# Performance work log

Hardware: AMD Instinct MI355X
Metric: run time of the kernel (lower is better)

The kernel has to match this reference:

```python
import jax, jax.numpy as jnp
import numpy as np

_N = 2048          # matrix_size (A_sparse.shape[0] in the original)
_NNZ = 32768       # number of factor / pred entries
_LOGCOND_EPS = 1e-12


def setup_inputs() -> dict:
    key = jax.random.key(0)
    k1, k2, k3, k4, k5 = jax.random.split(key, 5)
    pred_values = jax.random.normal(k1, (_NNZ,), dtype=jnp.float32)
    active_scales = jax.random.uniform(k2, (_NNZ,), dtype=jnp.float32) * 0.05
    A_factor = jax.random.normal(k3, (_N, _N), dtype=jnp.float32)
    factor_rows = jax.random.randint(k4, (_NNZ,), 0, _N, dtype=jnp.int32)
    factor_cols = jax.random.randint(k5, (_NNZ,), 0, _N, dtype=jnp.int32)
    return {
        "pred_values": pred_values,
        "active_scales": active_scales,
        "A_factor": A_factor,
        "factor_rows": factor_rows,
        "factor_cols": factor_cols,
    }


def reference(pred_values, active_scales, A_factor, factor_rows, factor_cols):
    n = A_factor.shape[0]
    dt = pred_values.dtype
    # SPD system matrix A (stands in for the original fixed A_sparse)
    A = A_factor @ A_factor.T / jnp.asarray(n, dt) + jnp.eye(n, dtype=dt)
    # Sparse factor L assembled from predicted values (scatter-add, dup-safe),
    # unit diagonal keeps L A L^T well conditioned / SPD.
    L = jnp.eye(n, dtype=dt).at[factor_rows, factor_cols].add(pred_values * active_scales)
    # Preconditioned matrix M = L A L^T (symmetric PSD)
    M = L @ A @ L.T
    M = 0.5 * (M + M.T)
    evals = jnp.linalg.eigvalsh(M)  # ascending
    lam_min = jnp.maximum(evals[0], _LOGCOND_EPS)
    lam_max = jnp.maximum(evals[-1], _LOGCOND_EPS)
    # loss = log(lambda_max) - log(lambda_min) = log condition number
    return jnp.log(lam_max) - jnp.log(lam_min)
```

## Files before the change

### kernel.cpp

```cpp
#include <hip/hip_runtime.h>

#define N2 2048
#define NNZ 32768
#define LK 22
#define NBL 128
#define BINCAP 64

typedef __attribute__((ext_vector_type(8))) _Float16 half8;
typedef __attribute__((ext_vector_type(4))) float f32x4;

#define AGENT __HIP_MEMORY_SCOPE_AGENT
#define AS1C(p) ((const __attribute__((address_space(1))) unsigned int*)(p))
#define AS3(p)  ((__attribute__((address_space(3))) unsigned int*)(p))

__device__ __forceinline__ unsigned short f2h(float f) {
  _Float16 h = (_Float16)f;
  return *(unsigned short*)&h;
}


__global__ __launch_bounds__(256) void convert_kernel(const float* __restrict__ W,
                                                      unsigned short* __restrict__ Hf,
                                                      unsigned* __restrict__ cntR,
                                                      unsigned* __restrict__ cntC) {
  if (blockIdx.x < 8)       cntR[blockIdx.x * 256 + threadIdx.x] = 0;
  else if (blockIdx.x < 16) cntC[(blockIdx.x - 8) * 256 + threadIdx.x] = 0;
  int i4 = blockIdx.x * 256 + threadIdx.x;
  float4 w = ((const float4*)W)[i4];
  ushort4 h;
  h.x = f2h(w.x); h.y = f2h(w.y); h.z = f2h(w.z); h.w = f2h(w.w);
  ((ushort4*)Hf)[i4] = h;
}

__global__ __launch_bounds__(256) void fill_kernel(const float* __restrict__ pred,
                                                   const float* __restrict__ scal,
                                                   const int* __restrict__ rows,
                                                   const int* __restrict__ cols,
                                                   unsigned* __restrict__ cntR,
                                                   int* __restrict__ binRc,
                                                   float* __restrict__ binRv,
                                                   unsigned* __restrict__ cntC,
                                                   int* __restrict__ binCr,
                                                   float* __restrict__ binCv) {
  int k = blockIdx.x * 256 + threadIdx.x;
  int r = rows[k], c = cols[k];
  float v = pred[k] * scal[k];
  unsigned pR = atomicAdd(&cntR[r], 1u);
  if (pR < BINCAP) { binRc[r * BINCAP + pR] = c; binRv[r * BINCAP + pR] = v; }
  unsigned pC = atomicAdd(&cntC[c], 1u);
  if (pC < BINCAP) { binCr[c * BINCAP + pC] = r; binCv[c * BINCAP + pC] = v; }
}

__global__ __launch_bounds__(256) void gatherG_kernel(const unsigned* __restrict__ cntR,
                                                      const int* __restrict__ binRc,
                                                      const float* __restrict__ binRv,
                                                      const unsigned short* __restrict__ Hf,
                                                      unsigned short* __restrict__ Gh) {
  const int r = blockIdx.x, tid = threadIdx.x;
  __shared__ int scol_[BINCAP];
  __shared__ float sval_[BINCAP];
  const unsigned ne = min(cntR[r], (unsigned)BINCAP);
  if (tid < ne) {
    scol_[tid] = binRc[r * BINCAP + tid];
    sval_[tid] = binRv[r * BINCAP + tid];
  }
  __syncthreads();
  uint4 own = *(const uint4*)(Hf + (size_t)r * 2048 + tid * 8);
  half8 ho = *(half8*)&own;
  float acc[8];
#pragma unroll
  for (int k = 0; k < 8; ++k) acc[k] = (float)ho[k];
  unsigned e = 0;
  for (; e + 8 <= ne; e += 8) {
    uint4 q[8];
#pragma unroll
    for (int u = 0; u < 8; ++u)
      q[u] = *(const uint4*)(Hf + (size_t)scol_[e + u] * 2048 + tid * 8);
#pragma unroll
    for (int u = 0; u < 8; ++u) {
      half8 hv = *(half8*)&q[u];
      const float v = sval_[e + u];
#pragma unroll
      for (int k = 0; k < 8; ++k) acc[k] += v * (float)hv[k];
    }
  }
  for (; e + 4 <= ne; e += 4) {
    uint4 q[4];
#pragma unroll
    for (int u = 0; u < 4; ++u)
      q[u] = *(const uint4*)(Hf + (size_t)scol_[e + u] * 2048 + tid * 8);
#pragma unroll
    for (int u = 0; u < 4; ++u) {
      half8 hv = *(half8*)&q[u];
      const float v = sval_[e + u];
#pragma unroll
      for (int k = 0; k < 8; ++k) acc[k] += v * (float)hv[k];
    }
  }
  for (; e < ne; ++e) {
    uint4 qq = *(const uint4*)(Hf + (size_t)scol_[e] * 2048 + tid * 8);
    half8 hv = *(half8*)&qq;
    const float v = sval_[e];
#pragma unroll
    for (int k = 0; k < 8; ++k) acc[k] += v * (float)hv[k];
  }
  unsigned short o[8];
#pragma unroll
  for (int k = 0; k < 8; ++k) o[k] = f2h(acc[k]);
  *(uint4*)(Gh + (size_t)r * 2048 + tid * 8) = *(uint4*)o;
}

__device__ __forceinline__ void stageXY(const unsigned short* __restrict__ Gh,
                                        char* Xb, char* Yb,
                                        int row0, int col0, int k0,
                                        int w, int lane) {
  const int srcc = ((lane & 7) * 16) ^ ((lane >> 3) << 4);
#pragma unroll
  for (int q = 0; q < 2; ++q) {
    const int rl = w * 16 + q * 8 + (lane >> 3);
    __builtin_amdgcn_global_load_lds(
        AS1C((const char*)(Gh + (size_t)(row0 + rl) * 2048 + k0) + srcc),
        AS3(Xb + (w * 16 + q * 8) * 128), 16, 0, 0);
    __builtin_amdgcn_global_load_lds(
        AS1C((const char*)(Gh + (size_t)(col0 + rl) * 2048 + k0) + srcc),
        AS3(Yb + (w * 16 + q * 8) * 128), 16, 0, 0);
  }
}

__global__ __launch_bounds__(512) void gemmM_kernel(const unsigned short* __restrict__ Gh,
                                                    float* __restrict__ M) {
  const int tid = threadIdx.x;
  int bi, bj;
  bool diag;
  if (blockIdx.x < 16) {
    bi = bj = blockIdx.x; diag = true;
  } else {
    int idx = blockIdx.x - 16;
    int j = 0;
    while (j < 15) {
      int offn = 15 * (j + 1) - (j + 1) * j / 2;
      if (idx < offn) break;
      ++j;
    }
    bj = j;
    int off = 15 * j - j * (j - 1) / 2;
    bi = j + 1 + (idx - off);
    diag = false;
  }

  __shared__ __align__(16) char smem[65536];
  float* LDSf = (float*)smem;

  const int w = tid >> 6, lane = tid & 63;
  const int row0 = bi * 128, col0 = bj * 128;
  const int mrow = lane & 15;
  const int crow = (lane >> 4) * 4, ccol = lane & 15;
  f32x4 acc[8];
#pragma unroll
  for (int n = 0; n < 8; ++n) acc[n] = (f32x4){0.f, 0.f, 0.f, 0.f};

  stageXY(Gh, smem, smem + 32768, row0, col0, 0, w, lane);

  const int arow = w * 16 + mrow;
  const int xswA = (mrow & 7) << 4;
  for (int t = 0; t < 32; ++t) {
    __syncthreads();
    if (t < 31)
      stageXY(Gh, smem + ((t + 1) & 1) * 16384, smem + 32768 + ((t + 1) & 1) * 16384,
              row0, col0, (t + 1) * 64, w, lane);
    const char* Xb = smem + (t & 1) * 16384;
    const char* Yb = smem + 32768 + (t & 1) * 16384;
#pragma unroll
    for (int kk = 0; kk < 2; ++kk) {
      const int cb = kk * 64 + (lane >> 4) * 16;
      half8 af = *(const half8*)(Xb + arow * 128 + (cb ^ xswA));
#pragma unroll
      for (int nt = 0; nt < 8; ++nt) {
        const int nrow = nt * 16 + mrow;
        half8 bf = *(const half8*)(Yb + nrow * 128 + (cb ^ ((nrow & 7) << 4)));
        acc[nt] = __builtin_amdgcn_mfma_f32_16x16x32_f16(af, bf, acc[nt], 0, 0, 0);
      }
    }
  }
  const float invn = 1.0f / 2048.0f;
  float vals[8][4];
#pragma unroll
  for (int nt = 0; nt < 8; ++nt) {
    const int gj = col0 + nt * 16 + ccol;
#pragma unroll
    for (int r = 0; r < 4; ++r) {
      const int gi = row0 + w * 16 + crow + r;
      float v = acc[nt][r] * invn + ((gi == gj) ? 1.0f : 0.0f);
      vals[nt][r] = v;
      M[(size_t)gi * 2048 + gj] = v;
    }
  }
  if (!diag) {
    __syncthreads();
    for (int round = 0; round < 2; ++round) {
      if ((w >> 2) == round) {
        float* myc = LDSf + (w & 3) * (16 * 132);
#pragma unroll
        for (int nt = 0; nt < 8; ++nt)
#pragma unroll
          for (int r = 0; r < 4; ++r)
            myc[(crow + r) * 132 + nt * 16 + ccol] = vals[nt][r];
        for (int u = 0; u < 32; ++u) {
          const int jj = u * 4 + (lane >> 4);
          const int ii = lane & 15;
          M[(size_t)(col0 + jj) * 2048 + row0 + w * 16 + ii] = myc[ii * 132 + jj];
        }
      }
      __syncthreads();
    }
  }
}

__device__ __forceinline__ float block_sum8(float v, float* red) {
#pragma unroll
  for (int off = 32; off; off >>= 1) v += __shfl_down(v, off);
  if ((threadIdx.x & 63) == 0) red[threadIdx.x >> 6] = v;
  __syncthreads();
  float r = ((red[0] + red[1]) + (red[2] + red[3])) +
            ((red[4] + red[5]) + (red[6] + red[7]));
  __syncthreads();
  return r;
}

__global__ __launch_bounds__(512) void lanczos_kernel(const float* __restrict__ M,
                                                      const unsigned* __restrict__ cntR,
                                                      const int* __restrict__ binRc,
                                                      const float* __restrict__ binRv,
                                                      const unsigned* __restrict__ cntC,
                                                      const int* __restrict__ binCr,
                                                      const float* __restrict__ binCv,
                                                      unsigned long long* __restrict__ Z0,
                                                      unsigned long long* __restrict__ Z1,
                                                      float* __restrict__ out) {
  const int tid = threadIdx.x, b = blockIdx.x;
  const int wave = tid >> 6, lane = tid & 63;
  __shared__ __align__(16) float Mlds[16 * 2048];
  __shared__ __align__(16) float VA[2048];
  __shared__ __align__(16) float VB[2048];
  __shared__ float red[8];
  __shared__ float al[LK + 2], b2[LK + 2];
  __shared__ float bnds[2], res[2];

  const float* Mblk = M + (size_t)b * 16 * 2048;
#pragma unroll
  for (int q = 0; q < 16; ++q)
    __builtin_amdgcn_global_load_lds(AS1C(Mblk + wave * 4096 + q * 256 + lane * 4),
                                     AS3(Mlds + wave * 4096 + q * 256), 16, 0, 0);

  float pv[4];
  float part = 0.f;
#pragma unroll
  for (int t = 0; t < 4; ++t) {
    int i = t * 512 + tid;
    unsigned u = (unsigned)i * 2654435761u;
    u ^= u >> 16; u *= 2246822519u; u ^= u >> 13;
    float rv = (float)(u >> 8) * (2.f / 16777216.f) - 1.f;
    pv[t] = rv;
    part += rv * rv;
  }
  float nrm = block_sum8(part, red);
  float innm = rsqrtf(nrm);
#pragma unroll
  for (int t = 0; t < 4; ++t) {
    int i = t * 512 + tid;
    VA[i] = pv[t] * innm;
    VB[i] = 0.f;
  }
  __syncthreads();

  for (int rr = 0; rr < 2; ++rr) {
    const int r = b * 16 + wave * 2 + rr;
    float* Mrow = Mlds + (wave * 2 + rr) * 2048;
    const unsigned nR = min(cntR[r], (unsigned)BINCAP);
    const unsigned nC = min(cntC[r], (unsigned)BINCAP);
    int c_ = 0; float v_ = 0.f; unsigned n_ = 0;
    if (lane < nR) {
      c_ = binRc[r * BINCAP + lane];
      v_ = binRv[r * BINCAP + lane];
      n_ = min(cntC[c_], (unsigned)BINCAP);
    }
    if (lane < nR) atomicAdd(&Mrow[c_], v_);
    if (lane < nC)
      atomicAdd(&Mrow[binCr[r * BINCAP + lane]], binCv[r * BINCAP + lane]);
    const unsigned g = lane >> 4, p0 = lane & 15;
    for (unsigned e = g; e < nR; e += 4) {
      const int c = __shfl(c_, (int)e);
      const float v = __shfl(v_, (int)e);
      const unsigned n2 = __shfl(n_, (int)e);
      for (unsigned p = p0; p < n2; p += 16)
        atomicAdd(&Mrow[binCr[c * BINCAP + p]], v * binCv[c * BINCAP + p]);
    }
  }
  __syncthreads();

  float* Vcur = VA;
  float* Vprev = VB;
  float beta_prev = 0.f;

  for (int j = 1; j <= LK; ++j) {
    unsigned long long* Z = (j & 1) ? Z0 : Z1;
#pragma unroll
    for (int rr = 0; rr < 2; ++rr) {
      const int r = b * 16 + wave * 2 + rr;
      const float4* Mr = (const float4*)(Mlds + (wave * 2 + rr) * 2048);
      float s = 0.f;
#pragma unroll
      for (int t = 0; t < 8; ++t) {
        int idx = t * 64 + lane;
        float4 m4 = Mr[idx];
        float4 v4 = ((const float4*)Vcur)[idx];
        s += m4.x * v4.x + m4.y * v4.y + m4.z * v4.z + m4.w * v4.w;
      }
#pragma unroll
      for (int off = 32; off; off >>= 1) s += __shfl_down(s, off);
      if (lane == 0) {
        float zv = s - beta_prev * Vprev[r];
        unsigned long long pk = ((unsigned long long)(unsigned)j << 32) |
                                (unsigned long long)(unsigned)__float_as_uint(zv);
        __hip_atomic_store(&Z[r], pk, __ATOMIC_RELAXED, AGENT);
      }
    }

    float va[4];
#pragma unroll
    for (int t = 0; t < 4; ++t) va[t] = Vcur[t * 512 + tid];

    unsigned long long w4[4];
    int rounds = 0;
    for (;;) {
      bool ok = true;
#pragma unroll
      for (int t = 0; t < 4; ++t) {
        w4[t] = __hip_atomic_load(&Z[t * 512 + tid], __ATOMIC_RELAXED, AGENT);
        ok &= ((unsigned)(w4[t] >> 32) == (unsigned)j);
      }
      if (ok) break;
      if (rounds == 1)      __builtin_amdgcn_s_sleep(1);
      else if (rounds == 2) __builtin_amdgcn_s_sleep(2);
      else if (rounds >= 3) __builtin_amdgcn_s_sleep(8);
      ++rounds;
    }
    float za[4];
    float pa = 0.f;
#pragma unroll
    for (int t = 0; t < 4; ++t) {
      za[t] = __uint_as_float((unsigned)w4[t]);
      pa += za[t] * va[t];
    }
    float alpha = block_sum8(pa, red);
    float pb = 0.f;
#pragma unroll
    for (int t = 0; t < 4; ++t) {
      float rsd = za[t] - alpha * va[t];
      pb += rsd * rsd;
    }
    float beta2 = block_sum8(pb, red);
    float beta = sqrtf(fmaxf(beta2, 1e-30f));
    float invb = 1.f / beta;
    if (tid == 0) { al[j] = alpha; b2[j] = beta2; }
#pragma unroll
    for (int t = 0; t < 4; ++t) {
      int i = t * 512 + tid;
      Vprev[i] = (za[t] - alpha * va[t]) * invb;
    }
    float* tmp = Vprev; Vprev = Vcur; Vcur = tmp;
    beta_prev = beta;
    __syncthreads();
  }

  if (b == 0) {
    if (tid == 0) {
      float lo = 1e30f, hi = -1e30f;
      for (int i = 1; i <= LK; ++i) {
        float bl = (i > 1) ? sqrtf(b2[i - 1]) : 0.f;
        float br = (i < LK) ? sqrtf(b2[i]) : 0.f;
        lo = fminf(lo, al[i] - bl - br);
        hi = fmaxf(hi, al[i] + bl + br);
      }
      bnds[0] = lo; bnds[1] = hi;
    }
    __syncthreads();
    if (wave < 2) {
      const int tcount = (wave == 0) ? 1 : LK;
      float lo = bnds[0], hi = bnds[1];
      for (int round = 0; round < 4; ++round) {
        float x = lo + (hi - lo) * (float)(lane + 1) * (1.f / 65.f);
        int cnt = 0;
        float d = al[1] - x;
        if (fabsf(d) < 1e-25f) d = -1e-25f;
        if (d < 0.f) cnt++;
        for (int i = 2; i <= LK; ++i) {
          d = (al[i] - x) - b2[i - 1] / d;
          if (fabsf(d) < 1e-25f) d = -1e-25f;
          if (d < 0.f) cnt++;
        }
        bool ab = (cnt >= tcount);
        float cand_hi = ab ? x : hi;
        float cand_lo = ab ? lo : x;
#pragma unroll
        for (int off = 32; off; off >>= 1) {
          cand_hi = fminf(cand_hi, __shfl_down(cand_hi, off));
          cand_lo = fmaxf(cand_lo, __shfl_down(cand_lo, off));
        }
        cand_hi = __shfl(cand_hi, 0);
        cand_lo = __shfl(cand_lo, 0);
        hi = cand_hi;
        lo = fminf(cand_lo, hi);
      }
      if (lane == 0) res[wave] = 0.5f * (lo + hi);
    }
    __syncthreads();
    if (tid == 0) {
      float lmin = fmaxf(res[0], 1e-12f);
      float lmax = fmaxf(res[1], 1e-12f);
      out[0] = logf(lmax) - logf(lmin);
    }
  }
}

extern "C" void kernel_launch(void* const* d_in, const int* in_sizes, int n_in,
                              void* d_out, int out_size, void* d_ws, size_t ws_size,
                              hipStream_t stream) {
  const float* pred = (const float*)d_in[0];
  const float* scal = (const float*)d_in[1];
  const float* W    = (const float*)d_in[2];
  const int*   rows = (const int*)d_in[3];
  const int*   cols = (const int*)d_in[4];
  float* out = (float*)d_out;

  char* ws = (char*)d_ws;
  const size_t MB = 1024 * 1024;
  unsigned short* Hf = (unsigned short*)(ws);
  unsigned short* Gh = (unsigned short*)(ws + 8 * MB);
  float* M = (float*)(ws + 16 * MB);
  char* ctrl = ws + 32 * MB;
  unsigned* cntR = (unsigned*)(ctrl);
  unsigned* cntC = (unsigned*)(ctrl + 8192);
  int*      binRc = (int*)(ctrl + 16384);
  float*    binRv = (float*)(ctrl + 16384 + 524288);
  int*      binCr = (int*)(ctrl + 16384 + 2 * 524288);
  float*    binCv = (float*)(ctrl + 16384 + 3 * 524288);
  unsigned long long* Z0 = (unsigned long long*)(ctrl + 16384 + 4 * 524288);
  unsigned long long* Z1 = (unsigned long long*)(ctrl + 16384 + 4 * 524288 + 16384);

  convert_kernel<<<4096, 256, 0, stream>>>(W, Hf, cntR, cntC);
  fill_kernel<<<NNZ / 256, 256, 0, stream>>>(pred, scal, rows, cols,
                                             cntR, binRc, binRv, cntC, binCr, binCv);
  gatherG_kernel<<<2048, 256, 0, stream>>>(cntR, binRc, binRv, Hf, Gh);
  gemmM_kernel<<<136, 512, 0, stream>>>(Gh, M);
  lanczos_kernel<<<NBL, 512, 0, stream>>>(M, cntR, binRc, binRv,
                                          cntC, binCr, binCv, Z0, Z1, out);
}
```

Before: 245.4 us.

## Fuse all five stages into one cooperative persistent kernel with grid syncs

Replaces the five separate launches (convert, bin fill, sparse gather, MFMA GEMM, Lanczos) with a single cooperative kernel of 256 blocks that runs each stage in turn, separated by grid.sync(). The intent is to remove per-launch overhead and inter-kernel gaps. In exchange, the convert and gather stages run at lower parallelism (8 rows per block instead of one block per row), and every block carries the large Lanczos LDS allocation, which limits occupancy for the early stages. Cooperative launch also requires that all 256 blocks be resident at once.

```diff
diff --git a/kernel.cpp b/kernel.cpp
--- a/kernel.cpp
+++ b/kernel.cpp
@@ -1,9 +1,11 @@
 #include <hip/hip_runtime.h>
+#include <hip/hip_cooperative_groups.h>
+
+namespace cg = cooperative_groups;
 
 #define N2 2048
 #define NNZ 32768
 #define LK 22
-#define NBL 128
 #define BINCAP 64
 
 typedef __attribute__((ext_vector_type(8))) _Float16 half8;
@@ -18,97 +20,6 @@
   return *(unsigned short*)&h;
 }
 
-
-__global__ __launch_bounds__(256) void convert_kernel(const float* __restrict__ W,
-                                                      unsigned short* __restrict__ Hf,
-                                                      unsigned* __restrict__ cntR,
-                                                      unsigned* __restrict__ cntC) {
-  if (blockIdx.x < 8)       cntR[blockIdx.x * 256 + threadIdx.x] = 0;
-  else if (blockIdx.x < 16) cntC[(blockIdx.x - 8) * 256 + threadIdx.x] = 0;
-  int i4 = blockIdx.x * 256 + threadIdx.x;
-  float4 w = ((const float4*)W)[i4];
-  ushort4 h;
-  h.x = f2h(w.x); h.y = f2h(w.y); h.z = f2h(w.z); h.w = f2h(w.w);
-  ((ushort4*)Hf)[i4] = h;
-}
-
-__global__ __launch_bounds__(256) void fill_kernel(const float* __restrict__ pred,
-                                                   const float* __restrict__ scal,
-                                                   const int* __restrict__ rows,
-                                                   const int* __restrict__ cols,
-                                                   unsigned* __restrict__ cntR,
-                                                   int* __restrict__ binRc,
-                                                   float* __restrict__ binRv,
-                                                   unsigned* __restrict__ cntC,
-                                                   int* __restrict__ binCr,
-                                                   float* __restrict__ binCv) {
-  int k = blockIdx.x * 256 + threadIdx.x;
-  int r = rows[k], c = cols[k];
-  float v = pred[k] * scal[k];
-  unsigned pR = atomicAdd(&cntR[r], 1u);
-  if (pR < BINCAP) { binRc[r * BINCAP + pR] = c; binRv[r * BINCAP + pR] = v; }
-  unsigned pC = atomicAdd(&cntC[c], 1u);
-  if (pC < BINCAP) { binCr[c * BINCAP + pC] = r; binCv[c * BINCAP + pC] = v; }
-}
-
-__global__ __launch_bounds__(256) void gatherG_kernel(const unsigned* __restrict__ cntR,
-                                                      const int* __restrict__ binRc,
-                                                      const float* __restrict__ binRv,
-                                                      const unsigned short* __restrict__ Hf,
-                                                      unsigned short* __restrict__ Gh) {
-  const int r = blockIdx.x, tid = threadIdx.x;
-  __shared__ int scol_[BINCAP];
-  __shared__ float sval_[BINCAP];
-  const unsigned ne = min(cntR[r], (unsigned)BINCAP);
-  if (tid < ne) {
-    scol_[tid] = binRc[r * BINCAP + tid];
-    sval_[tid] = binRv[r * BINCAP + tid];
-  }
-  __syncthreads();
-  uint4 own = *(const uint4*)(Hf + (size_t)r * 2048 + tid * 8);
-  half8 ho = *(half8*)&own;
-  float acc[8];
-#pragma unroll
-  for (int k = 0; k < 8; ++k) acc[k] = (float)ho[k];
-  unsigned e = 0;
-  for (; e + 8 <= ne; e += 8) {
-    uint4 q[8];
-#pragma unroll
-    for (int u = 0; u < 8; ++u)
-      q[u] = *(const uint4*)(Hf + (size_t)scol_[e + u] * 2048 + tid * 8);
-#pragma unroll
-    for (int u = 0; u < 8; ++u) {
-      half8 hv = *(half8*)&q[u];
-      const float v = sval_[e + u];
-#pragma unroll
-      for (int k = 0; k < 8; ++k) acc[k] += v * (float)hv[k];
-    }
-  }
-  for (; e + 4 <= ne; e += 4) {
-    uint4 q[4];
-#pragma unroll
-    for (int u = 0; u < 4; ++u)
-      q[u] = *(const uint4*)(Hf + (size_t)scol_[e + u] * 2048 + tid * 8);
-#pragma unroll
-    for (int u = 0; u < 4; ++u) {
-      half8 hv = *(half8*)&q[u];
-      const float v = sval_[e + u];
-#pragma unroll
-      for (int k = 0; k < 8; ++k) acc[k] += v * (float)hv[k];
-    }
-  }
-  for (; e < ne; ++e) {
-    uint4 qq = *(const uint4*)(Hf + (size_t)scol_[e] * 2048 + tid * 8);
-    half8 hv = *(half8*)&qq;
-    const float v = sval_[e];
-#pragma unroll
-    for (int k = 0; k < 8; ++k) acc[k] += v * (float)hv[k];
-  }
-  unsigned short o[8];
-#pragma unroll
-  for (int k = 0; k < 8; ++k) o[k] = f2h(acc[k]);
-  *(uint4*)(Gh + (size_t)r * 2048 + tid * 8) = *(uint4*)o;
-}
 
 __device__ __forceinline__ void stageXY(const unsigned short* __restrict__ Gh,
                                         char* Xb, char* Yb,
@@ -127,95 +38,6 @@
   }
 }
 
-__global__ __launch_bounds__(512) void gemmM_kernel(const unsigned short* __restrict__ Gh,
-                                                    float* __restrict__ M) {
-  const int tid = threadIdx.x;
-  int bi, bj;
-  bool diag;
-  if (blockIdx.x < 16) {
-    bi = bj = blockIdx.x; diag = true;
-  } else {
-    int idx = blockIdx.x - 16;
-    int j = 0;
-    while (j < 15) {
-      int offn = 15 * (j + 1) - (j + 1) * j / 2;
-      if (idx < offn) break;
-      ++j;
-    }
-    bj = j;
-    int off = 15 * j - j * (j - 1) / 2;
-    bi = j + 1 + (idx - off);
-    diag = false;
-  }
-
-  __shared__ __align__(16) char smem[65536];
-  float* LDSf = (float*)smem;
-
-  const int w = tid >> 6, lane = tid & 63;
-  const int row0 = bi * 128, col0 = bj * 128;
-  const int mrow = lane & 15;
-  const int crow = (lane >> 4) * 4, ccol = lane & 15;
-  f32x4 acc[8];
-#pragma unroll
-  for (int n = 0; n < 8; ++n) acc[n] = (f32x4){0.f, 0.f, 0.f, 0.f};
-
-  stageXY(Gh, smem, smem + 32768, row0, col0, 0, w, lane);
-
-  const int arow = w * 16 + mrow;
-  const int xswA = (mrow & 7) << 4;
-  for (int t = 0; t < 32; ++t) {
-    __syncthreads();
-    if (t < 31)
-      stageXY(Gh, smem + ((t + 1) & 1) * 16384, smem + 32768 + ((t + 1) & 1) * 16384,
-              row0, col0, (t + 1) * 64, w, lane);
-    const char* Xb = smem + (t & 1) * 16384;
-    const char* Yb = smem + 32768 + (t & 1) * 16384;
-#pragma unroll
-    for (int kk = 0; kk < 2; ++kk) {
-      const int cb = kk * 64 + (lane >> 4) * 16;
-      half8 af = *(const half8*)(Xb + arow * 128 + (cb ^ xswA));
-#pragma unroll
-      for (int nt = 0; nt < 8; ++nt) {
-        const int nrow = nt * 16 + mrow;
-        half8 bf = *(const half8*)(Yb + nrow * 128 + (cb ^ ((nrow & 7) << 4)));
-        acc[nt] = __builtin_amdgcn_mfma_f32_16x16x32_f16(af, bf, acc[nt], 0, 0, 0);
-      }
-    }
-  }
-  const float invn = 1.0f / 2048.0f;
-  float vals[8][4];
-#pragma unroll
-  for (int nt = 0; nt < 8; ++nt) {
-    const int gj = col0 + nt * 16 + ccol;
-#pragma unroll
-    for (int r = 0; r < 4; ++r) {
-      const int gi = row0 + w * 16 + crow + r;
-      float v = acc[nt][r] * invn + ((gi == gj) ? 1.0f : 0.0f);
-      vals[nt][r] = v;
-      M[(size_t)gi * 2048 + gj] = v;
-    }
-  }
-  if (!diag) {
-    __syncthreads();
-    for (int round = 0; round < 2; ++round) {
-      if ((w >> 2) == round) {
-        float* myc = LDSf + (w & 3) * (16 * 132);
-#pragma unroll
-        for (int nt = 0; nt < 8; ++nt)
-#pragma unroll
-          for (int r = 0; r < 4; ++r)
-            myc[(crow + r) * 132 + nt * 16 + ccol] = vals[nt][r];
-        for (int u = 0; u < 32; ++u) {
-          const int jj = u * 4 + (lane >> 4);
-          const int ii = lane & 15;
-          M[(size_t)(col0 + jj) * 2048 + row0 + w * 16 + ii] = myc[ii * 132 + jj];
-        }
-      }
-      __syncthreads();
-    }
-  }
-}
-
 __device__ __forceinline__ float block_sum8(float v, float* red) {
 #pragma unroll
   for (int off = 32; off; off >>= 1) v += __shfl_down(v, off);
@@ -227,24 +49,198 @@
   return r;
 }
 
-__global__ __launch_bounds__(512) void lanczos_kernel(const float* __restrict__ M,
-                                                      const unsigned* __restrict__ cntR,
-                                                      const int* __restrict__ binRc,
-                                                      const float* __restrict__ binRv,
-                                                      const unsigned* __restrict__ cntC,
-                                                      const int* __restrict__ binCr,
-                                                      const float* __restrict__ binCv,
-                                                      unsigned long long* __restrict__ Z0,
-                                                      unsigned long long* __restrict__ Z1,
-                                                      float* __restrict__ out) {
+__global__ __launch_bounds__(512) void mega_kernel(
+    const float* __restrict__ W, const float* __restrict__ pred,
+    const float* __restrict__ scal, const int* __restrict__ rows,
+    const int* __restrict__ cols,
+    unsigned short* __restrict__ Hf, unsigned short* __restrict__ Gh,
+    float* __restrict__ M,
+    unsigned* __restrict__ cntR, int* __restrict__ binRc, float* __restrict__ binRv,
+    unsigned* __restrict__ cntC, int* __restrict__ binCr, float* __restrict__ binCv,
+    unsigned long long* __restrict__ Z0, unsigned long long* __restrict__ Z1,
+    float* __restrict__ out) {
+  cg::grid_group grid = cg::this_grid();
   const int tid = threadIdx.x, b = blockIdx.x;
+  const int gid = b * 512 + tid;
   const int wave = tid >> 6, lane = tid & 63;
+
   __shared__ __align__(16) float Mlds[16 * 2048];
   __shared__ __align__(16) float VA[2048];
   __shared__ __align__(16) float VB[2048];
   __shared__ float red[8];
-  __shared__ float al[LK + 2], b2[LK + 2];
+  __shared__ float al[LK + 2], b2v[LK + 2];
   __shared__ float bnds[2], res[2];
+
+  if (gid < 2048)            cntR[gid] = 0;
+  else if (gid < 4096)       cntC[gid - 2048] = 0;
+  for (int i4 = gid; i4 < 1048576; i4 += 131072) {
+    float4 w4 = ((const float4*)W)[i4];
+    ushort4 h;
+    h.x = f2h(w4.x); h.y = f2h(w4.y); h.z = f2h(w4.z); h.w = f2h(w4.w);
+    ((ushort4*)Hf)[i4] = h;
+  }
+  grid.sync();
+
+  if (gid < NNZ) {
+    int r = rows[gid], c = cols[gid];
+    float v = pred[gid] * scal[gid];
+    unsigned pR = atomicAdd(&cntR[r], 1u);
+    if (pR < BINCAP) { binRc[r * BINCAP + pR] = c; binRv[r * BINCAP + pR] = v; }
+    unsigned pC = atomicAdd(&cntC[c], 1u);
+    if (pC < BINCAP) { binCr[c * BINCAP + pC] = r; binCv[c * BINCAP + pC] = v; }
+  }
+  grid.sync();
+
+  {
+    int* sc_ = (int*)VA;
+    float* sv_ = (float*)VB;
+    for (int it = 0; it < 4; ++it) {
+      const int sub = tid >> 8;
+      const int t2 = tid & 255;
+      const int r = b * 8 + it * 2 + sub;
+      int* sc = sc_ + sub * BINCAP;
+      float* sv = sv_ + sub * BINCAP;
+      const unsigned ne = min(cntR[r], (unsigned)BINCAP);
+      if (t2 < (int)ne) {
+        sc[t2] = binRc[r * BINCAP + t2];
+        sv[t2] = binRv[r * BINCAP + t2];
+      }
+      __syncthreads();
+      uint4 own = *(const uint4*)(Hf + (size_t)r * 2048 + t2 * 8);
+      half8 ho = *(half8*)&own;
+      float acc[8];
+#pragma unroll
+      for (int k = 0; k < 8; ++k) acc[k] = (float)ho[k];
+      unsigned e = 0;
+      for (; e + 8 <= ne; e += 8) {
+        uint4 q[8];
+#pragma unroll
+        for (int u = 0; u < 8; ++u)
+          q[u] = *(const uint4*)(Hf + (size_t)sc[e + u] * 2048 + t2 * 8);
+#pragma unroll
+        for (int u = 0; u < 8; ++u) {
+          half8 hv = *(half8*)&q[u];
+          const float v = sv[e + u];
+#pragma unroll
+          for (int k = 0; k < 8; ++k) acc[k] += v * (float)hv[k];
+        }
+      }
+      for (; e + 4 <= ne; e += 4) {
+        uint4 q[4];
+#pragma unroll
+        for (int u = 0; u < 4; ++u)
+          q[u] = *(const uint4*)(Hf + (size_t)sc[e + u] * 2048 + t2 * 8);
+#pragma unroll
+        for (int u = 0; u < 4; ++u) {
+          half8 hv = *(half8*)&q[u];
+          const float v = sv[e + u];
+#pragma unroll
+          for (int k = 0; k < 8; ++k) acc[k] += v * (float)hv[k];
+        }
+      }
+      for (; e < ne; ++e) {
+        uint4 qq = *(const uint4*)(Hf + (size_t)sc[e] * 2048 + t2 * 8);
+        half8 hv = *(half8*)&qq;
+        const float v = sv[e];
+#pragma unroll
+        for (int k = 0; k < 8; ++k) acc[k] += v * (float)hv[k];
+      }
+      unsigned short o[8];
+#pragma unroll
+      for (int k = 0; k < 8; ++k) o[k] = f2h(acc[k]);
+      *(uint4*)(Gh + (size_t)r * 2048 + t2 * 8) = *(uint4*)o;
+      __syncthreads();
+    }
+  }
+  grid.sync();
+
+  if (b < 136) {
+    char* smem = (char*)Mlds;
+    float* LDSf = (float*)smem;
+    int bi, bj;
+    bool diag;
+    if (b < 16) {
+      bi = bj = b; diag = true;
+    } else {
+      int idx = b - 16;
+      int j = 0;
+      while (j < 15) {
+        int offn = 15 * (j + 1) - (j + 1) * j / 2;
+        if (idx < offn) break;
+        ++j;
+      }
+      bj = j;
+      int off = 15 * j - j * (j - 1) / 2;
+      bi = j + 1 + (idx - off);
+      diag = false;
+    }
+    const int w = wave;
+    const int row0 = bi * 128, col0 = bj * 128;
+    const int mrow = lane & 15;
+    const int crow = (lane >> 4) * 4, ccol = lane & 15;
+    const int arow = w * 16 + mrow;
+    const int xswA = (mrow & 7) << 4;
+    f32x4 acc[8];
+#pragma unroll
+    for (int n = 0; n < 8; ++n) acc[n] = (f32x4){0.f, 0.f, 0.f, 0.f};
+
+    stageXY(Gh, smem, smem + 32768, row0, col0, 0, w, lane);
+    for (int t = 0; t < 32; ++t) {
+      __syncthreads();
+      if (t < 31)
+        stageXY(Gh, smem + ((t + 1) & 1) * 16384,
+                smem + 32768 + ((t + 1) & 1) * 16384,
+                row0, col0, (t + 1) * 64, w, lane);
+      const char* Xb = smem + (t & 1) * 16384;
+      const char* Yb = smem + 32768 + (t & 1) * 16384;
+#pragma unroll
+      for (int kk = 0; kk < 2; ++kk) {
+        const int cb = kk * 64 + (lane >> 4) * 16;
+        half8 af = *(const half8*)(Xb + arow * 128 + (cb ^ xswA));
+#pragma unroll
+        for (int nt = 0; nt < 8; ++nt) {
+          const int nrow = nt * 16 + mrow;
+          half8 bf = *(const half8*)(Yb + nrow * 128 + (cb ^ ((nrow & 7) << 4)));
+          acc[nt] = __builtin_amdgcn_mfma_f32_16x16x32_f16(af, bf, acc[nt], 0, 0, 0);
+        }
+      }
+    }
+    const float invn = 1.0f / 2048.0f;
+    float vals[8][4];
+#pragma unroll
+    for (int nt = 0; nt < 8; ++nt) {
+      const int gj = col0 + nt * 16 + ccol;
+#pragma unroll
+      for (int r = 0; r < 4; ++r) {
+        const int gi = row0 + w * 16 + crow + r;
+        float v = acc[nt][r] * invn + ((gi == gj) ? 1.0f : 0.0f);
+        vals[nt][r] = v;
+        M[(size_t)gi * 2048 + gj] = v;
+      }
+    }
+    if (!diag) {
+      __syncthreads();
+      for (int round = 0; round < 2; ++round) {
+        if ((w >> 2) == round) {
+          float* myc = LDSf + (w & 3) * (16 * 132);
+#pragma unroll
+          for (int nt = 0; nt < 8; ++nt)
+#pragma unroll
+            for (int r = 0; r < 4; ++r)
+              myc[(crow + r) * 132 + nt * 16 + ccol] = vals[nt][r];
+          for (int u = 0; u < 32; ++u) {
+            const int jj = u * 4 + (lane >> 4);
+            const int ii = lane & 15;
+            M[(size_t)(col0 + jj) * 2048 + row0 + w * 16 + ii] = myc[ii * 132 + jj];
+          }
+        }
+        __syncthreads();
+      }
+    }
+  }
+  grid.sync();
+
+  if (b >= 128) return;
 
   const float* Mblk = M + (size_t)b * 16 * 2048;
 #pragma unroll
@@ -279,13 +275,13 @@
     const unsigned nR = min(cntR[r], (unsigned)BINCAP);
     const unsigned nC = min(cntC[r], (unsigned)BINCAP);
     int c_ = 0; float v_ = 0.f; unsigned n_ = 0;
-    if (lane < nR) {
+    if (lane < (int)nR) {
       c_ = binRc[r * BINCAP + lane];
       v_ = binRv[r * BINCAP + lane];
       n_ = min(cntC[c_], (unsigned)BINCAP);
     }
-    if (lane < nR) atomicAdd(&Mrow[c_], v_);
-    if (lane < nC)
+    if (lane < (int)nR) atomicAdd(&Mrow[c_], v_);
+    if (lane < (int)nC)
       atomicAdd(&Mrow[binCr[r * BINCAP + lane]], binCv[r * BINCAP + lane]);
     const unsigned g = lane >> 4, p0 = lane & 15;
     for (unsigned e = g; e < nR; e += 4) {
@@ -362,7 +358,7 @@
     float beta2 = block_sum8(pb, red);
     float beta = sqrtf(fmaxf(beta2, 1e-30f));
     float invb = 1.f / beta;
-    if (tid == 0) { al[j] = alpha; b2[j] = beta2; }
+    if (tid == 0) { al[j] = alpha; b2v[j] = beta2; }
 #pragma unroll
     for (int t = 0; t < 4; ++t) {
       int i = t * 512 + tid;
@@ -377,8 +373,8 @@
     if (tid == 0) {
       float lo = 1e30f, hi = -1e30f;
       for (int i = 1; i <= LK; ++i) {
-        float bl = (i > 1) ? sqrtf(b2[i - 1]) : 0.f;
-        float br = (i < LK) ? sqrtf(b2[i]) : 0.f;
+        float bl = (i > 1) ? sqrtf(b2v[i - 1]) : 0.f;
+        float br = (i < LK) ? sqrtf(b2v[i]) : 0.f;
         lo = fminf(lo, al[i] - bl - br);
         hi = fmaxf(hi, al[i] + bl + br);
       }
@@ -395,7 +391,7 @@
         if (fabsf(d) < 1e-25f) d = -1e-25f;
         if (d < 0.f) cnt++;
         for (int i = 2; i <= LK; ++i) {
-          d = (al[i] - x) - b2[i - 1] / d;
+          d = (al[i] - x) - b2v[i - 1] / d;
           if (fabsf(d) < 1e-25f) d = -1e-25f;
           if (d < 0.f) cnt++;
         }
@@ -448,11 +444,13 @@
   unsigned long long* Z0 = (unsigned long long*)(ctrl + 16384 + 4 * 524288);
   unsigned long long* Z1 = (unsigned long long*)(ctrl + 16384 + 4 * 524288 + 16384);
 
-  convert_kernel<<<4096, 256, 0, stream>>>(W, Hf, cntR, cntC);
-  fill_kernel<<<NNZ / 256, 256, 0, stream>>>(pred, scal, rows, cols,
-                                             cntR, binRc, binRv, cntC, binCr, binCv);
-  gatherG_kernel<<<2048, 256, 0, stream>>>(cntR, binRc, binRv, Hf, Gh);
-  gemmM_kernel<<<136, 512, 0, stream>>>(Gh, M);
-  lanczos_kernel<<<NBL, 512, 0, stream>>>(M, cntR, binRc, binRv,
-                                          cntC, binCr, binCv, Z0, Z1, out);
+  void* kargs[] = {
+    (void*)&W, (void*)&pred, (void*)&scal, (void*)&rows, (void*)&cols,
+    (void*)&Hf, (void*)&Gh, (void*)&M,
+    (void*)&cntR, (void*)&binRc, (void*)&binRv,
+    (void*)&cntC, (void*)&binCr, (void*)&binCv,
+    (void*)&Z0, (void*)&Z1, (void*)&out
+  };
+  hipLaunchCooperativeKernel((const void*)mega_kernel, dim3(256), dim3(512),
+                             kargs, 0, stream);
 }
```

After: 382.2 us. 55.7% more time.
